# Performance work log

Hardware: AMD Instinct MI355X
Metric: run time of the kernel (lower is better)

Reference implementation:

```python
import jax, jax.numpy as jnp
import numpy as np

N_NODES = 50000
N_EDGES = 800000
IN = 64
HID = 64
OUT = 12
N_LAYERS = 4
N_GRAPHS = 512


def setup_inputs() -> dict:
    key = jax.random.key(0)
    ks = jax.random.split(key, 20)
    s = 1.0 / np.sqrt(HID)
    inp = {
        "x": jax.random.normal(ks[0], (N_NODES, IN), dtype=jnp.float32),
        "edge_index": jax.random.randint(ks[1], (2, N_EDGES), 0, N_NODES, dtype=jnp.int32),
        "batch": jnp.sort(jax.random.randint(ks[2], (N_NODES,), 0, N_GRAPHS, dtype=jnp.int32)),
        "batch_size": N_GRAPHS,
        # stacked per-layer ResGatedGraphConv params (in == hidden so one stack works)
        "Wk": jax.random.normal(ks[3], (N_LAYERS, HID, HID), dtype=jnp.float32) * s,
        "bk": jnp.zeros((N_LAYERS, HID), dtype=jnp.float32),
        "Wq": jax.random.normal(ks[4], (N_LAYERS, HID, HID), dtype=jnp.float32) * s,
        "bq": jnp.zeros((N_LAYERS, HID), dtype=jnp.float32),
        "Wv": jax.random.normal(ks[5], (N_LAYERS, HID, HID), dtype=jnp.float32) * s,
        "bv": jnp.zeros((N_LAYERS, HID), dtype=jnp.float32),
        "Ws": jax.random.normal(ks[6], (N_LAYERS, HID, HID), dtype=jnp.float32) * s,
        "bs": jnp.zeros((N_LAYERS, HID), dtype=jnp.float32),
        "mlp_w1": jax.random.normal(ks[7], (HID, HID), dtype=jnp.float32) * s,
        "mlp_b1": jnp.zeros((HID,), dtype=jnp.float32),
        "mlp_w2": jax.random.normal(ks[8], (HID, OUT), dtype=jnp.float32) * s,
        "mlp_b2": jnp.zeros((OUT,), dtype=jnp.float32),
    }
    return inp


def _res_gated_conv(x, src, dst, wk, bk_, wq, bq_, wv, bv_, ws, bs_, n_nodes):
    # PyG ResGatedGraphConv: eta = sigmoid(key(x_i) + query(x_j)); agg_i = sum eta * value(x_j)
    k = x @ wk + bk_  # [N, H]
    q = x @ wq + bq_
    v = x @ wv + bv_
    gate = jax.nn.sigmoid(k[dst] + q[src])          # [E, H] gather + elementwise
    msg = gate * v[src]                              # [E, H]
    agg = jax.ops.segment_sum(msg, dst, num_segments=n_nodes)  # scatter-add
    return agg + x @ ws + bs_                        # root/skip connection


def reference(x, edge_index, batch, batch_size, Wk, bk, Wq, bq, Wv, bv, Ws, bs,
              mlp_w1, mlp_b1, mlp_w2, mlp_b2):
    src, dst = edge_index[0], edge_index[1]  # messages flow src(j) -> dst(i)
    n_nodes = x.shape[0]
    for l in range(N_LAYERS):
        x = _res_gated_conv(x, src, dst, Wk[l], bk[l], Wq[l], bq[l],
                            Wv[l], bv[l], Ws[l], bs[l], n_nodes)
        x = jax.nn.gelu(x, approximate=False)  # torch nn.GELU default = exact
    # global mean pool over graphs
    sums = jax.ops.segment_sum(x, batch, num_segments=batch_size)          # [B, H]
    cnts = jax.ops.segment_sum(jnp.ones((n_nodes,), x.dtype), batch,
                               num_segments=batch_size)                    # [B]
    pooled = sums / jnp.maximum(cnts, 1.0)[:, None]
    # MLP head: Linear -> ReLU -> (dropout off at inference) -> Linear
    h = jax.nn.relu(pooled @ mlp_w1 + mlp_b1)
    return h @ mlp_w2 + mlp_b2
```

## Files before the change

### kernel.cpp

```cpp
#include <hip/hip_runtime.h>
#include <math.h>

#define N_NODES  50000
#define N_EDGES  800000
#define HID      64
#define OUT_DIM  12
#define N_LAYERS 4
#define N_GRAPHS 512

#define SCAN_CHUNK 512
#define N_CHUNKS   ((N_NODES + SCAN_CHUNK - 1) / SCAN_CHUNK)

typedef unsigned short u16;
typedef unsigned int   u32;
typedef __attribute__((ext_vector_type(8))) short bf16x8;
typedef __attribute__((ext_vector_type(4))) float f32x4;

__device__ __forceinline__ u32 f2bf(float f) {
    u32 u = __float_as_uint(f);
    return (u + 0x7FFFu + ((u >> 16) & 1u)) >> 16;
}
__device__ __forceinline__ float bf2f(u32 h) {
    return __uint_as_float(h << 16);
}

__global__ __launch_bounds__(256) void wprep_kernel(
    const float* __restrict__ Wq, const float* __restrict__ Wv,
    const float* __restrict__ Wk, const float* __restrict__ Ws,
    u16* __restrict__ wt)
{
    int m = blockIdx.x;
    int lyr = m >> 2, j = m & 3;
    const float* src;
    switch (j) { case 0: src = Wq; break; case 1: src = Wv; break;
                 case 2: src = Wk; break; default: src = Ws; }
    src += (size_t)lyr * HID * HID;
    int t  = threadIdx.x;
    int n  = t >> 2;
    int k0 = (t & 3) * 16;
    u32 buf[8];
    #pragma unroll
    for (int i = 0; i < 16; i += 2) {
        float f0 = src[(k0 + i) * HID + n];
        float f1 = src[(k0 + i + 1) * HID + n];
        buf[i / 2] = f2bf(f0) | (f2bf(f1) << 16);
    }
    u32* dst = (u32*)(wt + (size_t)m * 4096 + n * 64 + k0);
    *(uint4*)(dst)     = make_uint4(buf[0], buf[1], buf[2], buf[3]);
    *(uint4*)(dst + 4) = make_uint4(buf[4], buf[5], buf[6], buf[7]);
}

__global__ __launch_bounds__(256) void cvt_kernel(
    const float* __restrict__ x, u32* __restrict__ xbf)
{
    int i = blockIdx.x * 256 + threadIdx.x;
    if (i >= N_NODES * HID / 8) return;
    float4 a = ((const float4*)x)[2 * i];
    float4 b = ((const float4*)x)[2 * i + 1];
    ((uint4*)xbf)[i] = make_uint4(
        f2bf(a.x) | (f2bf(a.y) << 16), f2bf(a.z) | (f2bf(a.w) << 16),
        f2bf(b.x) | (f2bf(b.y) << 16), f2bf(b.z) | (f2bf(b.w) << 16));
}

__global__ __launch_bounds__(256) void gemm_mfma_kernel(
    const u16* __restrict__ xbf, const u16* __restrict__ wt, int layer,
    const float* __restrict__ bq, const float* __restrict__ bv,
    const float* __restrict__ bk, const float* __restrict__ bs,
    u32* __restrict__ qv, u32* __restrict__ kbf, float* __restrict__ os)
{
    const int t = threadIdx.x;
    const int w = t >> 6;
    const int l = t & 63;
    const int row16 = l & 15;
    const int kgrp  = l >> 4;
    const int gbase = blockIdx.x * 64;

    const u16 *wA, *wB; const float *bA, *bB;
    if (blockIdx.y == 0) { wA = wt + (size_t)(layer * 4 + 0) * 4096; bA = bq;
                           wB = wt + (size_t)(layer * 4 + 1) * 4096; bB = bv; }
    else                 { wA = wt + (size_t)(layer * 4 + 2) * 4096; bA = bk;
                           wB = wt + (size_t)(layer * 4 + 3) * 4096; bB = bs; }

    int nodeA = gbase + w * 16 + row16;
    int nodeAc = nodeA < N_NODES ? nodeA : N_NODES - 1;
    bf16x8 a0 = *(const bf16x8*)(xbf + (size_t)nodeAc * 64 + kgrp * 8);
    bf16x8 a1 = *(const bf16x8*)(xbf + (size_t)nodeAc * 64 + 32 + kgrp * 8);

    f32x4 acc[2][4];
    #pragma unroll
    for (int nt = 0; nt < 4; ++nt) {
        float fa = bA[nt * 16 + row16];
        float fb = bB[nt * 16 + row16];
        acc[0][nt] = (f32x4){fa, fa, fa, fa};
        acc[1][nt] = (f32x4){fb, fb, fb, fb};
    }

    #pragma unroll
    for (int nt = 0; nt < 4; ++nt) {
        const u16* pa = wA + (nt * 16 + row16) * 64 + kgrp * 8;
        const u16* pb = wB + (nt * 16 + row16) * 64 + kgrp * 8;
        bf16x8 ba0 = *(const bf16x8*)(pa);
        bf16x8 ba1 = *(const bf16x8*)(pa + 32);
        bf16x8 bb0 = *(const bf16x8*)(pb);
        bf16x8 bb1 = *(const bf16x8*)(pb + 32);
        acc[0][nt] = __builtin_amdgcn_mfma_f32_16x16x32_bf16(a0, ba0, acc[0][nt], 0, 0, 0);
        acc[0][nt] = __builtin_amdgcn_mfma_f32_16x16x32_bf16(a1, ba1, acc[0][nt], 0, 0, 0);
        acc[1][nt] = __builtin_amdgcn_mfma_f32_16x16x32_bf16(a0, bb0, acc[1][nt], 0, 0, 0);
        acc[1][nt] = __builtin_amdgcn_mfma_f32_16x16x32_bf16(a1, bb1, acc[1][nt], 0, 0, 0);
    }

    if (blockIdx.y == 0) {
        #pragma unroll
        for (int nt = 0; nt < 4; ++nt) {
            #pragma unroll
            for (int r = 0; r < 4; ++r) {
                float qe = acc[0][nt][r];
                float qo = __shfl_xor(qe, 1);
                float ve = acc[1][nt][r];
                float vo = __shfl_xor(ve, 1);
                if (!(l & 1)) {
                    int gn = gbase + w * 16 + kgrp * 4 + r;
                    if (gn < N_NODES) {
                        u32 qp = f2bf(qe) | (f2bf(qo) << 16);
                        u32 vp = f2bf(ve) | (f2bf(vo) << 16);
                        *(uint2*)(qv + (size_t)gn * 64 + nt * 16 + row16) = make_uint2(qp, vp);
                    }
                }
            }
        }
    } else {
        #pragma unroll
        for (int nt = 0; nt < 4; ++nt) {
            #pragma unroll
            for (int r = 0; r < 4; ++r) {
                float ke = acc[0][nt][r];
                float ko = __shfl_xor(ke, 1);
                int gn = gbase + w * 16 + kgrp * 4 + r;
                if (gn < N_NODES) {
                    int col = nt * 16 + row16;
                    os[(size_t)gn * 64 + col] = acc[1][nt][r];
                    if (!(l & 1))
                        kbf[(size_t)gn * 32 + (col >> 1)] = f2bf(ke) | (f2bf(ko) << 16);
                }
            }
        }
    }
}

__global__ __launch_bounds__(256) void hist_kernel(
    const int* __restrict__ ei, int* __restrict__ deg, int* __restrict__ rank)
{
    int e0 = (blockIdx.x * 256 + threadIdx.x) * 4;
    #pragma unroll
    for (int i = 0; i < 4; ++i) {
        int e = e0 + i;
        if (e < N_EDGES) rank[e] = atomicAdd(&deg[ei[N_EDGES + e]], 1);
    }
}

__global__ __launch_bounds__(SCAN_CHUNK) void scan1_kernel(
    const int* __restrict__ deg, int* __restrict__ base, int* __restrict__ blocksum)
{
    __shared__ int s[SCAN_CHUNK];
    int t = threadIdx.x;
    int i = blockIdx.x * SCAN_CHUNK + t;
    int v = (i < N_NODES) ? deg[i] : 0;
    s[t] = v;
    __syncthreads();
    for (int off = 1; off < SCAN_CHUNK; off <<= 1) {
        int u = (t >= off) ? s[t - off] : 0;
        __syncthreads();
        s[t] += u;
        __syncthreads();
    }
    if (i < N_NODES) base[i] = s[t] - v;
    if (t == SCAN_CHUNK - 1) blocksum[blockIdx.x] = s[t];
}

__global__ __launch_bounds__(128) void scan2_kernel(
    const int* __restrict__ blocksum, int* __restrict__ blockoff)
{
    __shared__ int s[128];
    int t = threadIdx.x;
    int v = (t < N_CHUNKS) ? blocksum[t] : 0;
    s[t] = v;
    __syncthreads();
    for (int off = 1; off < 128; off <<= 1) {
        int u = (t >= off) ? s[t - off] : 0;
        __syncthreads();
        s[t] += u;
        __syncthreads();
    }
    if (t < N_CHUNKS) blockoff[t] = s[t] - v;
}

__global__ __launch_bounds__(SCAN_CHUNK) void scan3_kernel(
    int* __restrict__ base, const int* __restrict__ blockoff)
{
    int i = blockIdx.x * SCAN_CHUNK + threadIdx.x;
    if (i < N_NODES) base[i] += blockoff[blockIdx.x];
    if (i == 0) base[N_NODES] = N_EDGES;
}

__global__ __launch_bounds__(256) void scatter_kernel(
    const int* __restrict__ ei, const int* __restrict__ base,
    const int* __restrict__ rank, int* __restrict__ csr_src)
{
    int e0 = (blockIdx.x * 256 + threadIdx.x) * 4;
    #pragma unroll
    for (int i = 0; i < 4; ++i) {
        int e = e0 + i;
        if (e < N_EDGES)
            csr_src[base[ei[N_EDGES + e]] + rank[e]] = ei[e];
    }
}

__global__ __launch_bounds__(256) void agg_gelu_kernel(
    const int* __restrict__ base, const int* __restrict__ csr_src,
    const u32* __restrict__ kbf, const u32* __restrict__ qv,
    const float* __restrict__ skip, u32* __restrict__ outxbf)
{
    int node = blockIdx.x * 4 + (threadIdx.x >> 6);
    if (node >= N_NODES) return;
    int lane = threadIdx.x & 63;
    int half = lane >> 5;
    int c    = lane & 31;

    u32 kp = kbf[(size_t)node * 32 + c];
    float kd0 = bf2f(kp & 0xffffu), kd1 = bf2f(kp >> 16);
    float acc0 = 0.f, acc1 = 0.f;
    int p0 = base[node];
    int p1 = base[node + 1];

    int p = p0 + half;
    for (; p + 6 < p1; p += 8) {
        int s0 = csr_src[p];
        int s1 = csr_src[p + 2];
        int s2 = csr_src[p + 4];
        int s3 = csr_src[p + 6];
        uint2 e0 = *(const uint2*)(qv + (size_t)s0 * 64 + 2 * c);
        uint2 e1 = *(const uint2*)(qv + (size_t)s1 * 64 + 2 * c);
        uint2 e2 = *(const uint2*)(qv + (size_t)s2 * 64 + 2 * c);
        uint2 e3 = *(const uint2*)(qv + (size_t)s3 * 64 + 2 * c);
        float g;
        g = 1.f / (1.f + __expf(-(kd0 + bf2f(e0.x & 0xffffu)))); acc0 = fmaf(g, bf2f(e0.y & 0xffffu), acc0);
        g = 1.f / (1.f + __expf(-(kd1 + bf2f(e0.x >> 16))));     acc1 = fmaf(g, bf2f(e0.y >> 16),     acc1);
        g = 1.f / (1.f + __expf(-(kd0 + bf2f(e1.x & 0xffffu)))); acc0 = fmaf(g, bf2f(e1.y & 0xffffu), acc0);
        g = 1.f / (1.f + __expf(-(kd1 + bf2f(e1.x >> 16))));     acc1 = fmaf(g, bf2f(e1.y >> 16),     acc1);
        g = 1.f / (1.f + __expf(-(kd0 + bf2f(e2.x & 0xffffu)))); acc0 = fmaf(g, bf2f(e2.y & 0xffffu), acc0);
        g = 1.f / (1.f + __expf(-(kd1 + bf2f(e2.x >> 16))));     acc1 = fmaf(g, bf2f(e2.y >> 16),     acc1);
        g = 1.f / (1.f + __expf(-(kd0 + bf2f(e3.x & 0xffffu)))); acc0 = fmaf(g, bf2f(e3.y & 0xffffu), acc0);
        g = 1.f / (1.f + __expf(-(kd1 + bf2f(e3.x >> 16))));     acc1 = fmaf(g, bf2f(e3.y >> 16),     acc1);
    }
    for (; p < p1; p += 2) {
        int s = csr_src[p];
        uint2 qp = *(const uint2*)(qv + (size_t)s * 64 + 2 * c);
        float g0 = 1.f / (1.f + __expf(-(kd0 + bf2f(qp.x & 0xffffu))));
        float g1 = 1.f / (1.f + __expf(-(kd1 + bf2f(qp.x >> 16))));
        acc0 = fmaf(g0, bf2f(qp.y & 0xffffu), acc0);
        acc1 = fmaf(g1, bf2f(qp.y >> 16), acc1);
    }

    acc0 += __shfl_xor(acc0, 32);
    acc1 += __shfl_xor(acc1, 32);

    if (half == 0) {
        float2 sk = *(const float2*)(skip + (size_t)node * HID + 2 * c);
        float xo0 = acc0 + sk.x;
        float xo1 = acc1 + sk.y;
        float g0 = 0.5f * xo0 * (1.f + erff(xo0 * 0.70710678118f));
        float g1 = 0.5f * xo1 * (1.f + erff(xo1 * 0.70710678118f));
        outxbf[(size_t)node * 32 + c] = f2bf(g0) | (f2bf(g1) << 16);
    }
}

__global__ __launch_bounds__(256) void bounds_kernel(
    const int* __restrict__ batch, int* __restrict__ start)
{
    int n = blockIdx.x * 256 + threadIdx.x;
    if (n >= N_NODES) return;
    int b  = batch[n];
    int bp = (n == 0) ? -1 : batch[n - 1];
    for (int g = bp + 1; g <= b; ++g) start[g] = n;
    if (n == N_NODES - 1) {
        for (int g = b + 1; g <= N_GRAPHS; ++g) start[g] = N_NODES;
    }
}

__global__ __launch_bounds__(256) void pool2_kernel(
    const u32* __restrict__ xbf, const int* __restrict__ start,
    float* __restrict__ pooled)
{
    int g   = blockIdx.x;
    int t   = threadIdx.x;
    int nid = t >> 5;
    int c   = t & 31;
    int s0 = start[g];
    int s1 = start[g + 1];
    float a0 = 0.f, a1 = 0.f;
    for (int n = s0 + nid; n < s1; n += 8) {
        u32 p = xbf[(size_t)n * 32 + c];
        a0 += bf2f(p & 0xffffu);
        a1 += bf2f(p >> 16);
    }
    __shared__ float red0[8][32], red1[8][32];
    red0[nid][c] = a0; red1[nid][c] = a1;
    __syncthreads();
    if (nid == 0) {
        float t0 = 0.f, t1 = 0.f;
        #pragma unroll
        for (int i = 0; i < 8; ++i) { t0 += red0[i][c]; t1 += red1[i][c]; }
        float cnt = fmaxf((float)(s1 - s0), 1.f);
        *(float2*)(pooled + (size_t)g * HID + 2 * c) = make_float2(t0 / cnt, t1 / cnt);
    }
}

__global__ __launch_bounds__(64) void head_kernel(
    const float* __restrict__ pooled,
    const float* __restrict__ w1, const float* __restrict__ b1,
    const float* __restrict__ w2, const float* __restrict__ b2,
    float* __restrict__ out)
{
    int g = blockIdx.x;
    int t = threadIdx.x;
    __shared__ float p[64];
    __shared__ float h[64];
    p[t] = pooled[(size_t)g * HID + t];
    __syncthreads();
    float acc = b1[t];
    #pragma unroll 8
    for (int k = 0; k < HID; ++k) acc = fmaf(p[k], w1[k * HID + t], acc);
    h[t] = fmaxf(acc, 0.f);
    __syncthreads();
    if (t < OUT_DIM) {
        float a2 = b2[t];
        #pragma unroll 8
        for (int k = 0; k < HID; ++k) a2 = fmaf(h[k], w2[k * OUT_DIM + t], a2);
        out[(size_t)g * OUT_DIM + t] = a2;
    }
}

extern "C" void kernel_launch(void* const* d_in, const int* in_sizes, int n_in,
                              void* d_out, int out_size, void* d_ws, size_t ws_size,
                              hipStream_t stream)
{
    const float* x     = (const float*)d_in[0];
    const int*   ei    = (const int*)d_in[1];
    const int*   batch = (const int*)d_in[2];
    const float* Wk = (const float*)d_in[4];
    const float* bk = (const float*)d_in[5];
    const float* Wq = (const float*)d_in[6];
    const float* bq = (const float*)d_in[7];
    const float* Wv = (const float*)d_in[8];
    const float* bv = (const float*)d_in[9];
    const float* Ws = (const float*)d_in[10];
    const float* bs = (const float*)d_in[11];
    const float* w1 = (const float*)d_in[12];
    const float* b1 = (const float*)d_in[13];
    const float* w2 = (const float*)d_in[14];
    const float* b2 = (const float*)d_in[15];
    float* out = (float*)d_out;

    char* wsb = (char*)d_ws;
    const size_t NF = (size_t)N_NODES * HID;
    u32*   xbf    = (u32*)wsb;                      wsb += NF * 2;
    u32*   bufK   = (u32*)wsb;                      wsb += NF * 2;
    float* bufS   = (float*)wsb;                    wsb += NF * 4;
    u32*   bufQV  = (u32*)wsb;                      wsb += NF * 4;
    u16*   wt     = (u16*)wsb;                      wsb += (size_t)16 * 4096 * 2;
    float* pooled = (float*)wsb;                    wsb += (size_t)N_GRAPHS * HID * 4;
    int*   baseI  = (int*)wsb;                      wsb += (N_NODES + 1) * 4;
    int*   csr_src= (int*)wsb;                      wsb += (size_t)N_EDGES * 4;
    int*   startI = (int*)wsb;                      wsb += (N_GRAPHS + 1) * 4;
    int* deg      = (int*)bufS;
    int* rank     = deg + N_NODES;
    int* blocksum = rank + N_EDGES;
    int* blockoff = blocksum + 128;

    const int gemm_gx = (N_NODES + 63) / 64;
    const int e4g     = (N_EDGES / 4 + 255) / 256;
    const int agg_gx  = (N_NODES + 3) / 4;
    const int nd_g    = (N_NODES + 255) / 256;
    const int cvt_g   = ((int)(NF / 8) + 255) / 256;

    hipMemsetAsync(deg, 0, (size_t)N_NODES * sizeof(int), stream);
    wprep_kernel<<<16, 256, 0, stream>>>(Wq, Wv, Wk, Ws, wt);
    cvt_kernel<<<cvt_g, 256, 0, stream>>>(x, xbf);
    hist_kernel<<<e4g, 256, 0, stream>>>(ei, deg, rank);
    scan1_kernel<<<N_CHUNKS, SCAN_CHUNK, 0, stream>>>(deg, baseI, blocksum);
    scan2_kernel<<<1, 128, 0, stream>>>(blocksum, blockoff);
    scan3_kernel<<<N_CHUNKS, SCAN_CHUNK, 0, stream>>>(baseI, blockoff);
    scatter_kernel<<<e4g, 256, 0, stream>>>(ei, baseI, rank, csr_src);
    bounds_kernel<<<nd_g, 256, 0, stream>>>(batch, startI);

    for (int l = 0; l < N_LAYERS; ++l) {
        gemm_mfma_kernel<<<dim3(gemm_gx, 2), 256, 0, stream>>>(
            (const u16*)xbf, wt, l,
            bq + (size_t)l * HID, bv + (size_t)l * HID,
            bk + (size_t)l * HID, bs + (size_t)l * HID,
            bufQV, bufK, bufS);
        agg_gelu_kernel<<<agg_gx, 256, 0, stream>>>(
            baseI, csr_src, bufK, bufQV, bufS, xbf);
    }

    pool2_kernel<<<N_GRAPHS, 256, 0, stream>>>(xbf, startI, pooled);
    head_kernel<<<N_GRAPHS, 64, 0, stream>>>(pooled, w1, b1, w2, b2, out);
}
```

Baseline: 339.3 us.

## Store skip in bf16, fold log2e into weights, merge GEMM grid halves

The skip projection is now written and read as packed bf16 instead of fp32, which halves that buffer's traffic between the GEMM and aggregation kernels. The Wq/Wk weights and biases are pre-scaled by log2(e), so the sigmoid can call exp2f directly instead of __expf. The GEMM launches one block per 64-node tile that computes all four projections, rather than splitting them across a second grid dimension, so each x tile is loaded once. The trade-offs are extra rounding on the skip path and higher register pressure in the GEMM from 16 accumulators.

```diff
diff --git a/kernel.cpp b/kernel.cpp
--- a/kernel.cpp
+++ b/kernel.cpp
@@ -16,12 +16,17 @@
 typedef __attribute__((ext_vector_type(8))) short bf16x8;
 typedef __attribute__((ext_vector_type(4))) float f32x4;
 
+#define L2E 1.44269504f
+
 __device__ __forceinline__ u32 f2bf(float f) {
     u32 u = __float_as_uint(f);
     return (u + 0x7FFFu + ((u >> 16) & 1u)) >> 16;
 }
 __device__ __forceinline__ float bf2f(u32 h) {
     return __uint_as_float(h << 16);
+}
+__device__ __forceinline__ float bf2f_hi(u32 h) {
+    return __uint_as_float(h & 0xffff0000u);
 }
 
 __global__ __launch_bounds__(256) void wprep_kernel(
@@ -35,14 +40,15 @@
     switch (j) { case 0: src = Wq; break; case 1: src = Wv; break;
                  case 2: src = Wk; break; default: src = Ws; }
     src += (size_t)lyr * HID * HID;
+    float scale = (j == 0 || j == 2) ? L2E : 1.0f;
     int t  = threadIdx.x;
     int n  = t >> 2;
     int k0 = (t & 3) * 16;
     u32 buf[8];
     #pragma unroll
     for (int i = 0; i < 16; i += 2) {
-        float f0 = src[(k0 + i) * HID + n];
-        float f1 = src[(k0 + i + 1) * HID + n];
+        float f0 = src[(k0 + i) * HID + n] * scale;
+        float f1 = src[(k0 + i + 1) * HID + n] * scale;
         buf[i / 2] = f2bf(f0) | (f2bf(f1) << 16);
     }
     u32* dst = (u32*)(wt + (size_t)m * 4096 + n * 64 + k0);
@@ -66,7 +72,7 @@
     const u16* __restrict__ xbf, const u16* __restrict__ wt, int layer,
     const float* __restrict__ bq, const float* __restrict__ bv,
     const float* __restrict__ bk, const float* __restrict__ bs,
-    u32* __restrict__ qv, u32* __restrict__ kbf, float* __restrict__ os)
+    u32* __restrict__ qv, u32* __restrict__ kbf, u32* __restrict__ sbf)
 {
     const int t = threadIdx.x;
     const int w = t >> 6;
@@ -75,73 +81,56 @@
     const int kgrp  = l >> 4;
     const int gbase = blockIdx.x * 64;
 
-    const u16 *wA, *wB; const float *bA, *bB;
-    if (blockIdx.y == 0) { wA = wt + (size_t)(layer * 4 + 0) * 4096; bA = bq;
-                           wB = wt + (size_t)(layer * 4 + 1) * 4096; bB = bv; }
-    else                 { wA = wt + (size_t)(layer * 4 + 2) * 4096; bA = bk;
-                           wB = wt + (size_t)(layer * 4 + 3) * 4096; bB = bs; }
+    const u16* wbase = wt + (size_t)layer * 4 * 4096;
 
     int nodeA = gbase + w * 16 + row16;
     int nodeAc = nodeA < N_NODES ? nodeA : N_NODES - 1;
     bf16x8 a0 = *(const bf16x8*)(xbf + (size_t)nodeAc * 64 + kgrp * 8);
     bf16x8 a1 = *(const bf16x8*)(xbf + (size_t)nodeAc * 64 + 32 + kgrp * 8);
 
-    f32x4 acc[2][4];
+    f32x4 acc[4][4];
     #pragma unroll
     for (int nt = 0; nt < 4; ++nt) {
-        float fa = bA[nt * 16 + row16];
-        float fb = bB[nt * 16 + row16];
-        acc[0][nt] = (f32x4){fa, fa, fa, fa};
-        acc[1][nt] = (f32x4){fb, fb, fb, fb};
-    }
-
-    #pragma unroll
-    for (int nt = 0; nt < 4; ++nt) {
-        const u16* pa = wA + (nt * 16 + row16) * 64 + kgrp * 8;
-        const u16* pb = wB + (nt * 16 + row16) * 64 + kgrp * 8;
-        bf16x8 ba0 = *(const bf16x8*)(pa);
-        bf16x8 ba1 = *(const bf16x8*)(pa + 32);
-        bf16x8 bb0 = *(const bf16x8*)(pb);
-        bf16x8 bb1 = *(const bf16x8*)(pb + 32);
-        acc[0][nt] = __builtin_amdgcn_mfma_f32_16x16x32_bf16(a0, ba0, acc[0][nt], 0, 0, 0);
-        acc[0][nt] = __builtin_amdgcn_mfma_f32_16x16x32_bf16(a1, ba1, acc[0][nt], 0, 0, 0);
-        acc[1][nt] = __builtin_amdgcn_mfma_f32_16x16x32_bf16(a0, bb0, acc[1][nt], 0, 0, 0);
-        acc[1][nt] = __builtin_amdgcn_mfma_f32_16x16x32_bf16(a1, bb1, acc[1][nt], 0, 0, 0);
-    }
-
-    if (blockIdx.y == 0) {
+        int col = nt * 16 + row16;
+        float fq = bq[col] * L2E;
+        float fv = bv[col];
+        float fk = bk[col] * L2E;
+        float fs = bs[col];
+        acc[0][nt] = (f32x4){fq, fq, fq, fq};
+        acc[1][nt] = (f32x4){fv, fv, fv, fv};
+        acc[2][nt] = (f32x4){fk, fk, fk, fk};
+        acc[3][nt] = (f32x4){fs, fs, fs, fs};
+    }
+
+    #pragma unroll
+    for (int m = 0; m < 4; ++m) {
         #pragma unroll
         for (int nt = 0; nt < 4; ++nt) {
-            #pragma unroll
-            for (int r = 0; r < 4; ++r) {
-                float qe = acc[0][nt][r];
-                float qo = __shfl_xor(qe, 1);
-                float ve = acc[1][nt][r];
-                float vo = __shfl_xor(ve, 1);
-                if (!(l & 1)) {
-                    int gn = gbase + w * 16 + kgrp * 4 + r;
-                    if (gn < N_NODES) {
-                        u32 qp = f2bf(qe) | (f2bf(qo) << 16);
-                        u32 vp = f2bf(ve) | (f2bf(vo) << 16);
-                        *(uint2*)(qv + (size_t)gn * 64 + nt * 16 + row16) = make_uint2(qp, vp);
-                    }
-                }
-            }
+            const u16* pb = wbase + m * 4096 + (nt * 16 + row16) * 64 + kgrp * 8;
+            bf16x8 b0 = *(const bf16x8*)(pb);
+            bf16x8 b1 = *(const bf16x8*)(pb + 32);
+            acc[m][nt] = __builtin_amdgcn_mfma_f32_16x16x32_bf16(a0, b0, acc[m][nt], 0, 0, 0);
+            acc[m][nt] = __builtin_amdgcn_mfma_f32_16x16x32_bf16(a1, b1, acc[m][nt], 0, 0, 0);
         }
-    } else {
+    }
+
+    #pragma unroll
+    for (int nt = 0; nt < 4; ++nt) {
         #pragma unroll
-        for (int nt = 0; nt < 4; ++nt) {
-            #pragma unroll
-            for (int r = 0; r < 4; ++r) {
-                float ke = acc[0][nt][r];
-                float ko = __shfl_xor(ke, 1);
-                int gn = gbase + w * 16 + kgrp * 4 + r;
-                if (gn < N_NODES) {
-                    int col = nt * 16 + row16;
-                    os[(size_t)gn * 64 + col] = acc[1][nt][r];
-                    if (!(l & 1))
-                        kbf[(size_t)gn * 32 + (col >> 1)] = f2bf(ke) | (f2bf(ko) << 16);
-                }
+        for (int r = 0; r < 4; ++r) {
+            float qe = acc[0][nt][r]; float qo = __shfl_xor(qe, 1);
+            float ve = acc[1][nt][r]; float vo = __shfl_xor(ve, 1);
+            float ke = acc[2][nt][r]; float ko = __shfl_xor(ke, 1);
+            float se = acc[3][nt][r]; float so = __shfl_xor(se, 1);
+            int gn = gbase + w * 16 + kgrp * 4 + r;
+            if (!(l & 1) && gn < N_NODES) {
+                int col = nt * 16 + row16;
+                u32 qp = f2bf(qe) | (f2bf(qo) << 16);
+                u32 vp = f2bf(ve) | (f2bf(vo) << 16);
+                *(uint2*)(qv + (size_t)gn * 64 + col) = make_uint2(qp, vp);
+                int cp = col >> 1;
+                kbf[(size_t)gn * 32 + cp] = f2bf(ke) | (f2bf(ko) << 16);
+                sbf[(size_t)gn * 32 + cp] = f2bf(se) | (f2bf(so) << 16);
             }
         }
     }
@@ -218,7 +207,7 @@
 __global__ __launch_bounds__(256) void agg_gelu_kernel(
     const int* __restrict__ base, const int* __restrict__ csr_src,
     const u32* __restrict__ kbf, const u32* __restrict__ qv,
-    const float* __restrict__ skip, u32* __restrict__ outxbf)
+    const u32* __restrict__ sbf, u32* __restrict__ outxbf)
 {
     int node = blockIdx.x * 4 + (threadIdx.x >> 6);
     if (node >= N_NODES) return;
@@ -227,7 +216,7 @@
     int c    = lane & 31;
 
     u32 kp = kbf[(size_t)node * 32 + c];
-    float kd0 = bf2f(kp & 0xffffu), kd1 = bf2f(kp >> 16);
+    float kd0 = bf2f(kp & 0xffffu), kd1 = bf2f_hi(kp);
     float acc0 = 0.f, acc1 = 0.f;
     int p0 = base[node];
     int p1 = base[node + 1];
@@ -243,31 +232,31 @@
         uint2 e2 = *(const uint2*)(qv + (size_t)s2 * 64 + 2 * c);
         uint2 e3 = *(const uint2*)(qv + (size_t)s3 * 64 + 2 * c);
         float g;
-        g = 1.f / (1.f + __expf(-(kd0 + bf2f(e0.x & 0xffffu)))); acc0 = fmaf(g, bf2f(e0.y & 0xffffu), acc0);
-        g = 1.f / (1.f + __expf(-(kd1 + bf2f(e0.x >> 16))));     acc1 = fmaf(g, bf2f(e0.y >> 16),     acc1);
-        g = 1.f / (1.f + __expf(-(kd0 + bf2f(e1.x & 0xffffu)))); acc0 = fmaf(g, bf2f(e1.y & 0xffffu), acc0);
-        g = 1.f / (1.f + __expf(-(kd1 + bf2f(e1.x >> 16))));     acc1 = fmaf(g, bf2f(e1.y >> 16),     acc1);
-        g = 1.f / (1.f + __expf(-(kd0 + bf2f(e2.x & 0xffffu)))); acc0 = fmaf(g, bf2f(e2.y & 0xffffu), acc0);
-        g = 1.f / (1.f + __expf(-(kd1 + bf2f(e2.x >> 16))));     acc1 = fmaf(g, bf2f(e2.y >> 16),     acc1);
-        g = 1.f / (1.f + __expf(-(kd0 + bf2f(e3.x & 0xffffu)))); acc0 = fmaf(g, bf2f(e3.y & 0xffffu), acc0);
-        g = 1.f / (1.f + __expf(-(kd1 + bf2f(e3.x >> 16))));     acc1 = fmaf(g, bf2f(e3.y >> 16),     acc1);
+        g = 1.f / (1.f + exp2f(-(kd0 + bf2f(e0.x & 0xffffu)))); acc0 = fmaf(g, bf2f(e0.y & 0xffffu), acc0);
+        g = 1.f / (1.f + exp2f(-(kd1 + bf2f_hi(e0.x))));        acc1 = fmaf(g, bf2f_hi(e0.y),        acc1);
+        g = 1.f / (1.f + exp2f(-(kd0 + bf2f(e1.x & 0xffffu)))); acc0 = fmaf(g, bf2f(e1.y & 0xffffu), acc0);
+        g = 1.f / (1.f + exp2f(-(kd1 + bf2f_hi(e1.x))));        acc1 = fmaf(g, bf2f_hi(e1.y),        acc1);
+        g = 1.f / (1.f + exp2f(-(kd0 + bf2f(e2.x & 0xffffu)))); acc0 = fmaf(g, bf2f(e2.y & 0xffffu), acc0);
+        g = 1.f / (1.f + exp2f(-(kd1 + bf2f_hi(e2.x))));        acc1 = fmaf(g, bf2f_hi(e2.y),        acc1);
+        g = 1.f / (1.f + exp2f(-(kd0 + bf2f(e3.x & 0xffffu)))); acc0 = fmaf(g, bf2f(e3.y & 0xffffu), acc0);
+        g = 1.f / (1.f + exp2f(-(kd1 + bf2f_hi(e3.x))));        acc1 = fmaf(g, bf2f_hi(e3.y),        acc1);
     }
     for (; p < p1; p += 2) {
         int s = csr_src[p];
         uint2 qp = *(const uint2*)(qv + (size_t)s * 64 + 2 * c);
-        float g0 = 1.f / (1.f + __expf(-(kd0 + bf2f(qp.x & 0xffffu))));
-        float g1 = 1.f / (1.f + __expf(-(kd1 + bf2f(qp.x >> 16))));
+        float g0 = 1.f / (1.f + exp2f(-(kd0 + bf2f(qp.x & 0xffffu))));
+        float g1 = 1.f / (1.f + exp2f(-(kd1 + bf2f_hi(qp.x))));
         acc0 = fmaf(g0, bf2f(qp.y & 0xffffu), acc0);
-        acc1 = fmaf(g1, bf2f(qp.y >> 16), acc1);
+        acc1 = fmaf(g1, bf2f_hi(qp.y), acc1);
     }
 
     acc0 += __shfl_xor(acc0, 32);
     acc1 += __shfl_xor(acc1, 32);
 
     if (half == 0) {
-        float2 sk = *(const float2*)(skip + (size_t)node * HID + 2 * c);
-        float xo0 = acc0 + sk.x;
-        float xo1 = acc1 + sk.y;
+        u32 sp = sbf[(size_t)node * 32 + c];
+        float xo0 = acc0 + bf2f(sp & 0xffffu);
+        float xo1 = acc1 + bf2f_hi(sp);
         float g0 = 0.5f * xo0 * (1.f + erff(xo0 * 0.70710678118f));
         float g1 = 0.5f * xo1 * (1.f + erff(xo1 * 0.70710678118f));
         outxbf[(size_t)node * 32 + c] = f2bf(g0) | (f2bf(g1) << 16);
@@ -365,14 +354,14 @@
     const size_t NF = (size_t)N_NODES * HID;
     u32*   xbf    = (u32*)wsb;                      wsb += NF * 2;
     u32*   bufK   = (u32*)wsb;                      wsb += NF * 2;
-    float* bufS   = (float*)wsb;                    wsb += NF * 4;
+    u32*   bufSbf = (u32*)wsb;                      wsb += NF * 2;
     u32*   bufQV  = (u32*)wsb;                      wsb += NF * 4;
     u16*   wt     = (u16*)wsb;                      wsb += (size_t)16 * 4096 * 2;
     float* pooled = (float*)wsb;                    wsb += (size_t)N_GRAPHS * HID * 4;
     int*   baseI  = (int*)wsb;                      wsb += (N_NODES + 1) * 4;
     int*   csr_src= (int*)wsb;                      wsb += (size_t)N_EDGES * 4;
     int*   startI = (int*)wsb;                      wsb += (N_GRAPHS + 1) * 4;
-    int* deg      = (int*)bufS;
+    int* deg      = (int*)bufSbf;
     int* rank     = deg + N_NODES;
     int* blocksum = rank + N_EDGES;
     int* blockoff = blocksum + 128;
@@ -394,13 +383,13 @@
     bounds_kernel<<<nd_g, 256, 0, stream>>>(batch, startI);
 
     for (int l = 0; l < N_LAYERS; ++l) {
-        gemm_mfma_kernel<<<dim3(gemm_gx, 2), 256, 0, stream>>>(
+        gemm_mfma_kernel<<<gemm_gx, 256, 0, stream>>>(
             (const u16*)xbf, wt, l,
             bq + (size_t)l * HID, bv + (size_t)l * HID,
             bk + (size_t)l * HID, bs + (size_t)l * HID,
-            bufQV, bufK, bufS);
+            bufQV, bufK, bufSbf);
         agg_gelu_kernel<<<agg_gx, 256, 0, stream>>>(
-            baseI, csr_src, bufK, bufQV, bufS, xbf);
+            baseI, csr_src, bufK, bufQV, bufSbf, xbf);
     }
 
     pool2_kernel<<<N_GRAPHS, 256, 0, stream>>>(xbf, startI, pooled);
```

New measurement: 366.4 us. 8.0% more time.
